# Optimization experiments

Measured on AMD Instinct MI355X. Metric: run time of the kernel, lower is better.

The kernel has to match this reference:

```python
import jax, jax.numpy as jnp
import numpy as np

C = 256
LN_EPS = 1e-5
LEAKY_SLOPE = 0.01

def _layernorm(t, g, b):
    mu = jnp.mean(t, axis=-1, keepdims=True)
    var = jnp.mean((t - mu) ** 2, axis=-1, keepdims=True)
    return (t - mu) * jax.lax.rsqrt(var + LN_EPS) * g + b

def setup_inputs() -> dict:
    key = jax.random.key(0)
    ks = jax.random.split(key, 16)
    b, d, h, w = 4, 4096, 64, 64
    s = lambda n: 1.0 / np.sqrt(n)
    return {
        "x": jax.random.normal(ks[0], (b, 1, d), jnp.float32),
        "y": jax.random.normal(ks[1], (b, C, h, w), jnp.float32),
        "q_w": jax.random.normal(ks[2], (C, C), jnp.float32) * s(C),
        "q_b": jnp.zeros((C,), jnp.float32),
        "dw_w": jax.random.normal(ks[3], (C,), jnp.float32),
        "dw_b": jnp.zeros((C,), jnp.float32),
        "kv_w1": jax.random.normal(ks[4], (1, C // 2), jnp.float32),
        "kv_b1": jnp.zeros((C // 2,), jnp.float32),
        "ln1_g": jnp.ones((C // 2,), jnp.float32),
        "ln1_b": jnp.zeros((C // 2,), jnp.float32),
        "kv_w2": jax.random.normal(ks[5], (C // 2, C), jnp.float32) * s(C // 2),
        "kv_b2": jnp.zeros((C,), jnp.float32),
        "ln2_g": jnp.ones((C,), jnp.float32),
        "ln2_b": jnp.zeros((C,), jnp.float32),
        "kv_w3": jax.random.normal(ks[6], (C, C), jnp.float32) * s(C),
        "kv_b3": jnp.zeros((C,), jnp.float32),
        "ln3_g": jnp.ones((C,), jnp.float32),
        "ln3_b": jnp.zeros((C,), jnp.float32),
        "kv_w4": jax.random.normal(ks[7], (C, 2 * C), jnp.float32) * s(C),
        "kv_b4": jnp.zeros((2 * C,), jnp.float32),
        "proj_w": jax.random.normal(ks[8], (C, C), jnp.float32) * s(C),
        "proj_b": jnp.zeros((C,), jnp.float32),
    }

def reference(x, y, q_w, q_b, dw_w, dw_b, kv_w1, kv_b1, ln1_g, ln1_b,
              kv_w2, kv_b2, ln2_g, ln2_b, kv_w3, kv_b3, ln3_g, ln3_b,
              kv_w4, kv_b4, proj_w, proj_b):
    b, c, h, w = y.shape
    # x: [b, 1, d] -> [b, d, 1]; MLP kv-generator lifts each scalar to 2c channels
    t = jnp.swapaxes(x, 1, 2)  # [b, d, 1]
    t = jax.nn.leaky_relu(_layernorm(t @ kv_w1 + kv_b1, ln1_g, ln1_b), LEAKY_SLOPE)
    t = jax.nn.leaky_relu(_layernorm(t @ kv_w2 + kv_b2, ln2_g, ln2_b), LEAKY_SLOPE)
    t = jax.nn.leaky_relu(_layernorm(t @ kv_w3 + kv_b3, ln3_g, ln3_b), LEAKY_SLOPE)
    t = jax.nn.silu(t @ kv_w4 + kv_b4)  # [b, d, 2c]
    k, v = jnp.split(t, 2, axis=-1)  # each [b, d, c]
    k = jnp.swapaxes(k, 1, 2)  # [b, c, d]
    # q = dwconv1x1(conv1x1(y)): 1x1 conv is a channel matmul; depthwise 1x1 is per-channel affine
    q = jnp.einsum('bchw,oc->bohw', y, q_w) + q_b[None, :, None, None]
    q = q * dw_w[None, :, None, None] + dw_b[None, :, None, None]
    q = q.reshape(b, c, h * w).transpose(0, 2, 1)  # [b, hw, c]
    scores = jnp.einsum('bic,bcd->bid', q, k) * (float(c) ** -0.5)  # [b, hw, d]
    attn = jax.nn.softmax(scores, axis=2)
    h_ = jnp.einsum('bid,bdc->bic', attn, v)  # [b, hw, c]
    h_ = h_.transpose(0, 2, 1).reshape(b, c, h, w)
    h_ = jnp.einsum('bchw,oc->bohw', h_, proj_w) + proj_b[None, :, None, None]
    return y + h_
```

## Files before the change

kernel.cpp:

```cpp
#include <hip/hip_runtime.h>
#include <cstdint>
#include <cstddef>

using bf16   = __bf16;
using bf16x8 = __bf16 __attribute__((ext_vector_type(8)));
using f32x4  = float  __attribute__((ext_vector_type(4)));
using u16    = unsigned short;
using ushort8 = __attribute__((ext_vector_type(8))) unsigned short;

#define MFMA16(a, b, c) __builtin_amdgcn_mfma_f32_16x16x32_bf16(a, b, c, 0, 0, 0)

__device__ __forceinline__ u16 f2bf(float f) {
  union { float f; unsigned u; } v; v.f = f;
  unsigned r = v.u + 0x7fffu + ((v.u >> 16) & 1u);
  return (u16)(r >> 16);
}
__device__ __forceinline__ u16 bfc(float f) {
  union { float f; unsigned u; } v; v.f = f;
  return (u16)((v.u + 0x8000u) >> 16);
}
__device__ __forceinline__ float b2f(u16 h) {
  union { unsigned u; float f; } v; v.u = ((unsigned)h) << 16; return v.f;
}
__device__ __forceinline__ bf16x8 ldb8(const u16* p) { return *(const bf16x8*)p; }
__device__ __forceinline__ float red_sum16(float v) {
  v += __shfl_xor(v, 1, 64); v += __shfl_xor(v, 2, 64);
  v += __shfl_xor(v, 4, 64); v += __shfl_xor(v, 8, 64);
  return v;
}
__device__ __forceinline__ void gll16(const u16* g, u16* l) {
  __builtin_amdgcn_global_load_lds(
      (const __attribute__((address_space(1))) void*)g,
      (__attribute__((address_space(3))) void*)l, 16, 0, 0);
}

#define QSCALE 0.09016844005556021f

__global__ void k_prep(const float* __restrict__ kv_w2, const float* __restrict__ kv_w3,
                       const float* __restrict__ kv_w4, const float* __restrict__ q_w,
                       const float* __restrict__ proj_w,
                       u16* __restrict__ Wt2, u16* __restrict__ Wt3, u16* __restrict__ Wt4,
                       u16* __restrict__ Qw, u16* __restrict__ Pww) {
  int idx = blockIdx.x * 256 + threadIdx.x;
  if (idx < 32768) {
    int n = idx >> 7, k = idx & 127;
    Wt2[idx] = f2bf(kv_w2[k * 256 + n]);
  } else if (idx < 98304) {
    int j = idx - 32768, n = j >> 8, k = j & 255;
    Wt3[j] = f2bf(kv_w3[k * 256 + n]);
  } else if (idx < 229376) {
    int j = idx - 98304, n = j >> 8, k = j & 255;
    Wt4[j] = f2bf(kv_w4[k * 512 + n]);
  } else if (idx < 294912) {
    int j = idx - 229376;
    Qw[j] = f2bf(q_w[j]);
  } else if (idx < 360448) {
    int j = idx - 294912;
    Pww[j] = f2bf(proj_w[j]);
  }
}

__device__ __forceinline__ void ln_store(f32x4* acc, const float* __restrict__ bias,
    const float* __restrict__ g, const float* __restrict__ bb, u16* act,
    int w, int quad, int l16) {
  #pragma unroll
  for (int f = 0; f < 16; ++f) {
    float bv = bias[f * 16 + l16];
    acc[f][0] += bv; acc[f][1] += bv; acc[f][2] += bv; acc[f][3] += bv;
  }
  #pragma unroll
  for (int r = 0; r < 4; ++r) {
    float s = 0;
    #pragma unroll
    for (int f = 0; f < 16; ++f) s += acc[f][r];
    s = red_sum16(s);
    float mu = s * (1.f / 256.f);
    float vv = 0;
    #pragma unroll
    for (int f = 0; f < 16; ++f) { float d = acc[f][r] - mu; vv += d * d; }
    vv = red_sum16(vv);
    float inv = rsqrtf(vv * (1.f / 256.f) + 1e-5f);
    int rl = w * 16 + quad * 4 + r;
    #pragma unroll
    for (int f = 0; f < 16; ++f) {
      int col = f * 16 + l16;
      float o = (acc[f][r] - mu) * inv * g[col] + bb[col];
      o = o > 0.f ? o : 0.01f * o;
      act[rl * 264 + col] = f2bf(o);
    }
  }
}

template<int K>
__device__ __forceinline__ void mlp_layer(u16* act, u16* sW, const u16* __restrict__ Wt,
    const float* __restrict__ bias, const float* __restrict__ g, const float* __restrict__ bb,
    int tid, int w, int quad, int l16) {
  bf16x8 af[K / 32];
  #pragma unroll
  for (int kk = 0; kk < K / 32; ++kk) af[kk] = ldb8(act + (w * 16 + l16) * 264 + kk * 32 + quad * 8);
  f32x4 z = {0.f, 0.f, 0.f, 0.f};
  f32x4 acc[16];
  #pragma unroll
  for (int f = 0; f < 16; ++f) acc[f] = z;
  for (int nc = 0; nc < 8; ++nc) {
    __syncthreads();
    #pragma unroll
    for (int p = 0; p < K / 64; ++p) {
      int q = p * 256 + tid; int row = q / (K / 8), c8 = q % (K / 8);
      *(uint4*)(sW + row * 264 + c8 * 8) = *(const uint4*)(Wt + (size_t)(nc * 32 + row) * K + c8 * 8);
    }
    __syncthreads();
    #pragma unroll
    for (int nb = 0; nb < 2; ++nb) {
      int f = nc * 2 + nb;
      #pragma unroll
      for (int kk = 0; kk < K / 32; ++kk)
        acc[f] = MFMA16(af[kk], ldb8(sW + (nb * 16 + l16) * 264 + kk * 32 + quad * 8), acc[f]);
    }
  }
  ln_store(acc, bias, g, bb, act, w, quad, l16);
  __syncthreads();
}

__device__ __forceinline__ void mlp_layer4(u16* act, u16* sW, const u16* __restrict__ Wt4,
    const float* __restrict__ bias4, u16* __restrict__ Kt, u16* __restrict__ Vt,
    int i0, int tid, int w, int quad, int l16) {
  bf16x8 af[8];
  #pragma unroll
  for (int kk = 0; kk < 8; ++kk) af[kk] = ldb8(act + (w * 16 + l16) * 264 + kk * 32 + quad * 8);
  f32x4 z = {0.f, 0.f, 0.f, 0.f};
  for (int h = 0; h < 2; ++h) {
    f32x4 acc[16];
    #pragma unroll
    for (int f = 0; f < 16; ++f) acc[f] = z;
    for (int nc = 0; nc < 8; ++nc) {
      __syncthreads();
      #pragma unroll
      for (int p = 0; p < 4; ++p) {
        int q = p * 256 + tid; int row = q >> 5, c8 = q & 31;
        *(uint4*)(sW + row * 264 + c8 * 8) =
            *(const uint4*)(Wt4 + (size_t)(h * 256 + nc * 32 + row) * 256 + c8 * 8);
      }
      __syncthreads();
      #pragma unroll
      for (int nb = 0; nb < 2; ++nb) {
        int f = nc * 2 + nb;
        #pragma unroll
        for (int kk = 0; kk < 8; ++kk)
          acc[f] = MFMA16(af[kk], ldb8(sW + (nb * 16 + l16) * 264 + kk * 32 + quad * 8), acc[f]);
      }
    }
    #pragma unroll
    for (int f = 0; f < 16; ++f) {
      int col = f * 16 + l16;
      float bv = bias4[h * 256 + col];
      if (h == 0) {
        int chunk = f * 2 + (l16 >> 3), co = col & 7;
        #pragma unroll
        for (int r = 0; r < 4; ++r) {
          int rowg = i0 + w * 16 + quad * 4 + r;
          float v = acc[f][r] + bv;
          v = v / (1.f + __expf(-v));
          int chs = (chunk + (rowg & 31)) & 31;
          Kt[(size_t)rowg * 256 + chs * 8 + co] = f2bf(v);
        }
      } else {
        int rowg0 = i0 + w * 16 + quad * 4;
        int bb2 = rowg0 >> 12, d0 = rowg0 & 4095;
        int dd = d0 & 31, qd = dd >> 3;
        int chs = (qd + (col & 3) + ((col >> 2) & 3)) & 3;
        ushort4 u;
        #pragma unroll
        for (int r = 0; r < 4; ++r) {
          float v = acc[f][r] + bv;
          v = v / (1.f + __expf(-v));
          ((u16*)&u)[r] = f2bf(v);
        }
        size_t off = ((size_t)(bb2 * 128 + (d0 >> 5)) * 8192) + col * 32 + chs * 8 + (dd & 7);
        *(ushort4*)(Vt + off) = u;
      }
    }
  }
}

__global__ __launch_bounds__(256, 2) void k_fused(
    const float* __restrict__ x, const float* __restrict__ w1, const float* __restrict__ bias1,
    const float* __restrict__ g1, const float* __restrict__ bb1,
    const u16* __restrict__ Wt2, const float* __restrict__ bias2,
    const float* __restrict__ g2, const float* __restrict__ bb2,
    const u16* __restrict__ Wt3, const float* __restrict__ bias3,
    const float* __restrict__ g3, const float* __restrict__ bb3,
    const u16* __restrict__ Wt4, const float* __restrict__ bias4,
    const float* __restrict__ y, const u16* __restrict__ Qw,
    const float* __restrict__ qb, const float* __restrict__ dww, const float* __restrict__ dwb,
    u16* __restrict__ Kt, u16* __restrict__ Vt, u16* __restrict__ Qb) {
  __shared__ __align__(16) u16 smem[25344];
  int tid = threadIdx.x, w = tid >> 6, lane = tid & 63, quad = lane >> 4, l16 = lane & 15;

  if (blockIdx.x < 256) {
    u16* act = smem;
    u16* sW  = smem + 16896;
    int i0 = blockIdx.x * 64;
    {
      int rloc = w * 16 + (lane >> 2);
      int c0 = (lane & 3) * 32;
      float xv = x[i0 + rloc];
      float t[32];
      float s = 0.f;
      #pragma unroll
      for (int j = 0; j < 32; ++j) { t[j] = xv * w1[c0 + j] + bias1[c0 + j]; s += t[j]; }
      s += __shfl_xor(s, 1, 64); s += __shfl_xor(s, 2, 64);
      float mu = s * (1.f / 128.f);
      float vv = 0.f;
      #pragma unroll
      for (int j = 0; j < 32; ++j) { float d = t[j] - mu; vv += d * d; }
      vv += __shfl_xor(vv, 1, 64); vv += __shfl_xor(vv, 2, 64);
      float inv = rsqrtf(vv * (1.f / 128.f) + 1e-5f);
      #pragma unroll
      for (int jo = 0; jo < 4; ++jo) {
        ushort8 pk;
        #pragma unroll
        for (int e = 0; e < 8; ++e) {
          int j = jo * 8 + e;
          float o = (t[j] - mu) * inv * g1[c0 + j] + bb1[c0 + j];
          o = o > 0.f ? o : 0.01f * o;
          pk[e] = f2bf(o);
        }
        *(ushort8*)(act + rloc * 264 + c0 + jo * 8) = pk;
      }
    }
    __syncthreads();
    mlp_layer<128>(act, sW, Wt2, bias2, g2, bb2, tid, w, quad, l16);
    mlp_layer<256>(act, sW, Wt3, bias3, g3, bb3, tid, w, quad, l16);
    mlp_layer4(act, sW, Wt4, bias4, Kt, Vt, i0, tid, w, quad, l16);
    return;
  }

  u16* sY = smem;
  u16* sB = smem + 4608;
  int t = blockIdx.x - 256;
  int b = t >> 6, i0 = (t & 63) * 64;
  f32x4 z = {0.f, 0.f, 0.f, 0.f};
  f32x4 acc[16];
  #pragma unroll
  for (int f = 0; f < 16; ++f) acc[f] = z;
  for (int kc = 0; kc < 4; ++kc) {
    if (kc) __syncthreads();
    {
      int cl = tid >> 4;
      int il = (tid & 15) * 4;
      #pragma unroll
      for (int p = 0; p < 4; ++p) {
        int c = kc * 64 + p * 16 + cl;
        float4 v = *(const float4*)(y + ((size_t)(b * 256 + c)) * 4096 + i0 + il);
        sY[(il + 0) * 72 + p * 16 + cl] = f2bf(v.x);
        sY[(il + 1) * 72 + p * 16 + cl] = f2bf(v.y);
        sY[(il + 2) * 72 + p * 16 + cl] = f2bf(v.z);
        sY[(il + 3) * 72 + p * 16 + cl] = f2bf(v.w);
      }
    }
    #pragma unroll
    for (int p = 0; p < 8; ++p) {
      int q = p * 256 + tid; int row = q >> 3, k8 = q & 7;
      *(uint4*)(sB + row * 72 + k8 * 8) = *(const uint4*)(Qw + (size_t)row * 256 + kc * 64 + k8 * 8);
    }
    __syncthreads();
    #pragma unroll
    for (int kk = 0; kk < 2; ++kk) {
      bf16x8 af = ldb8(sY + (w * 16 + l16) * 72 + kk * 32 + quad * 8);
      #pragma unroll
      for (int f = 0; f < 16; ++f) {
        bf16x8 bfr = ldb8(sB + (f * 16 + l16) * 72 + kk * 32 + quad * 8);
        acc[f] = MFMA16(af, bfr, acc[f]);
      }
    }
  }
  #pragma unroll
  for (int f = 0; f < 16; ++f) {
    int col = f * 16 + l16;
    float q0 = qb[col], sc = dww[col], dB = dwb[col];
    #pragma unroll
    for (int r = 0; r < 4; ++r) {
      int rowg = i0 + w * 16 + quad * 4 + r;
      float v = ((acc[f][r] + q0) * sc + dB) * QSCALE;
      Qb[((size_t)(b * 4096 + rowg)) * 256 + col] = f2bf(v);
    }
  }
}

__global__ __launch_bounds__(256, 2) void k_attn(const u16* __restrict__ Qb, const u16* __restrict__ Kt,
    const u16* __restrict__ Vt, u16* __restrict__ Op, float* __restrict__ Ol) {
  __shared__ __align__(16) u16 smem[37888];
  int tid = threadIdx.x, w = tid >> 6, lane = tid & 63, quad = lane >> 4, l16 = lane & 15;
  int b = blockIdx.x & 3, kh = (blockIdx.x >> 2) & 3, qt = blockIdx.x >> 4;
  int i0 = qt * 128 + w * 32;

  bf16x8 qf[2][8];
  {
    const u16* qrow = Qb + ((size_t)(b * 4096 + i0 + l16)) * 256 + quad * 8;
    #pragma unroll
    for (int kk = 0; kk < 8; ++kk) {
      qf[0][kk] = ldb8(qrow + kk * 32);
      qf[1][kk] = ldb8(qrow + 16 * 256 + kk * 32);
    }
  }
  f32x4 z = {0.f, 0.f, 0.f, 0.f};
  f32x4 oacc[2][16];
  #pragma unroll
  for (int sub = 0; sub < 2; ++sub)
    #pragma unroll
    for (int f = 0; f < 16; ++f) oacc[sub][f] = z;
  float l4[2][4] = {{0.f, 0.f, 0.f, 0.f}, {0.f, 0.f, 0.f, 0.f}};

  u16* sPw = smem + 32768 + w * 1280;
  int wp = w & 1;
  const u16* gSrc = ((w < 2) ? Kt : Vt) + ((size_t)(b * 128 + kh * 32) * 8192) + wp * 4096 + lane * 8;
  u16* lBase = smem + ((w < 2) ? 0 : 8192) + wp * 4096 + lane * 8;

  #pragma unroll
  for (int i = 0; i < 8; ++i) gll16(gSrc + i * 512, lBase + i * 512);
  gSrc += 8192;

  #pragma unroll 1
  for (int kt = 0; kt < 32; ++kt) {
    int buf = kt & 1;
    const u16* sK = smem + buf * 16384;
    const u16* sV = sK + 8192;
    asm volatile("s_waitcnt vmcnt(0)" ::: "memory");
    __syncthreads();
    if (kt < 31) {
      u16* dst = lBase + (buf ^ 1) * 16384;
      #pragma unroll
      for (int i = 0; i < 8; ++i) gll16(gSrc + i * 512, dst + i * 512);
      gSrc += 8192;
    }
    f32x4 s00 = z, s01 = z, s10 = z, s11 = z;
    #pragma unroll
    for (int kk = 0; kk < 8; ++kk) {
      int ch0 = (kk * 4 + quad + l16) & 31;
      int ch1 = (ch0 + 16) & 31;
      bf16x8 k0 = ldb8(sK + l16 * 256 + ch0 * 8);
      bf16x8 k1 = ldb8(sK + (16 + l16) * 256 + ch1 * 8);
      s00 = MFMA16(qf[0][kk], k0, s00);
      s01 = MFMA16(qf[0][kk], k1, s01);
      s10 = MFMA16(qf[1][kk], k0, s10);
      s11 = MFMA16(qf[1][kk], k1, s11);
    }
    #pragma unroll
    for (int r = 0; r < 4; ++r) {
      float p0 = exp2f(s00[r]);
      float p1 = exp2f(s01[r]);
      float p2 = exp2f(s10[r]);
      float p3 = exp2f(s11[r]);
      l4[0][r] += p0 + p1;
      l4[1][r] += p2 + p3;
      int row0 = (quad * 4 + r) * 40;
      sPw[row0 + l16]            = bfc(p0);
      sPw[row0 + 16 + l16]       = bfc(p1);
      sPw[640 + row0 + l16]      = bfc(p2);
      sPw[640 + row0 + 16 + l16] = bfc(p3);
    }
    asm volatile("s_waitcnt lgkmcnt(0)" ::: "memory");
    bf16x8 pf0 = ldb8(sPw + l16 * 40 + quad * 8);
    bf16x8 pf1 = ldb8(sPw + 640 + l16 * 40 + quad * 8);
    #pragma unroll
    for (int f = 0; f < 16; ++f) {
      int c = f * 16 + l16;
      int chs = (quad + (c & 3) + ((c >> 2) & 3)) & 3;
      bf16x8 vf = ldb8(sV + c * 32 + chs * 8);
      oacc[0][f] = MFMA16(pf0, vf, oacc[0][f]);
      oacc[1][f] = MFMA16(pf1, vf, oacc[1][f]);
    }
  }
  #pragma unroll
  for (int sub = 0; sub < 2; ++sub)
    #pragma unroll
    for (int r = 0; r < 4; ++r) l4[sub][r] = red_sum16(l4[sub][r]);
  #pragma unroll
  for (int sub = 0; sub < 2; ++sub)
    #pragma unroll
    for (int r = 0; r < 4; ++r) {
      size_t gr = (size_t)kh * 16384 + b * 4096 + i0 + sub * 16 + quad * 4 + r;
      u16* orow = Op + gr * 256;
      #pragma unroll
      for (int f = 0; f < 16; ++f) orow[f * 16 + l16] = f2bf(oacc[sub][f][r]);
      if (l16 == 0) Ol[gr] = l4[sub][r];
    }
}

__global__ __launch_bounds__(256) void k_proj(const u16* __restrict__ Op, const float* __restrict__ Ol,
    const u16* __restrict__ Pw, const float* __restrict__ pb, const float* __restrict__ y,
    float* __restrict__ out) {
  __shared__ u16 sA[64 * 136];
  __shared__ u16 sB[64 * 136];
  __shared__ float sW[64];
  int tid = threadIdx.x, w = tid >> 6, lane = tid & 63, quad = lane >> 4, l16 = lane & 15;
  int i0 = blockIdx.x * 64, o0 = blockIdx.y * 64, b = blockIdx.z;
  if (tid < 64) {
    size_t gr = (size_t)b * 4096 + i0 + tid;
    float L = Ol[gr] + Ol[gr + 16384] + Ol[gr + 32768] + Ol[gr + 49152];
    sW[tid] = 1.f / L;
  }
  __syncthreads();
  f32x4 z = {0.f, 0.f, 0.f, 0.f};
  f32x4 acc[4] = {z, z, z, z};
  for (int kc = 0; kc < 2; ++kc) {
    if (kc) __syncthreads();
    #pragma unroll
    for (int p = 0; p < 4; ++p) {
      int q = p * 256 + tid; int row = q >> 4, c8 = q & 15;
      *(uint4*)(sA + row * 136 + c8 * 8) = *(const uint4*)(Pw + ((size_t)(o0 + row)) * 256 + kc * 128 + c8 * 8);
      size_t gr = (size_t)b * 4096 + i0 + row;
      const u16* hp = Op + gr * 256 + kc * 128 + c8 * 8;
      uint4 u0 = *(const uint4*)(hp);
      uint4 u1 = *(const uint4*)(hp + 4194304);
      uint4 u2 = *(const uint4*)(hp + 8388608);
      uint4 u3 = *(const uint4*)(hp + 12582912);
      float wr = sW[row];
      const u16* p0 = (const u16*)&u0; const u16* p1 = (const u16*)&u1;
      const u16* p2 = (const u16*)&u2; const u16* p3 = (const u16*)&u3;
      ushort8 ov;
      #pragma unroll
      for (int e = 0; e < 8; ++e) {
        float v = (b2f(p0[e]) + b2f(p1[e]) + b2f(p2[e]) + b2f(p3[e])) * wr;
        ov[e] = f2bf(v);
      }
      *(ushort8*)(sB + row * 136 + c8 * 8) = ov;
    }
    __syncthreads();
    #pragma unroll
    for (int kk = 0; kk < 4; ++kk) {
      bf16x8 af = ldb8(sA + (w * 16 + l16) * 136 + kk * 32 + quad * 8);
      #pragma unroll
      for (int nb = 0; nb < 4; ++nb) {
        bf16x8 bfr = ldb8(sB + (nb * 16 + l16) * 136 + kk * 32 + quad * 8);
        acc[nb] = MFMA16(af, bfr, acc[nb]);
      }
    }
  }
  #pragma unroll
  for (int nb = 0; nb < 4; ++nb) {
    #pragma unroll
    for (int r = 0; r < 4; ++r) {
      int og = o0 + w * 16 + quad * 4 + r;
      size_t idx = ((size_t)(b * 256 + og)) * 4096 + i0 + nb * 16 + l16;
      out[idx] = y[idx] + acc[nb][r] + pb[og];
    }
  }
}

extern "C" void kernel_launch(void* const* d_in, const int* in_sizes, int n_in,
                              void* d_out, int out_size, void* d_ws, size_t ws_size,
                              hipStream_t stream) {
  (void)in_sizes; (void)n_in; (void)out_size; (void)ws_size;
  const float* x     = (const float*)d_in[0];
  const float* y     = (const float*)d_in[1];
  const float* q_w   = (const float*)d_in[2];
  const float* q_b   = (const float*)d_in[3];
  const float* dw_w  = (const float*)d_in[4];
  const float* dw_b  = (const float*)d_in[5];
  const float* kv_w1 = (const float*)d_in[6];
  const float* kv_b1 = (const float*)d_in[7];
  const float* ln1_g = (const float*)d_in[8];
  const float* ln1_b = (const float*)d_in[9];
  const float* kv_w2 = (const float*)d_in[10];
  const float* kv_b2 = (const float*)d_in[11];
  const float* ln2_g = (const float*)d_in[12];
  const float* ln2_b = (const float*)d_in[13];
  const float* kv_w3 = (const float*)d_in[14];
  const float* kv_b3 = (const float*)d_in[15];
  const float* ln3_g = (const float*)d_in[16];
  const float* ln3_b = (const float*)d_in[17];
  const float* kv_w4 = (const float*)d_in[18];
  const float* kv_b4 = (const float*)d_in[19];
  const float* proj_w = (const float*)d_in[20];
  const float* proj_b = (const float*)d_in[21];
  float* out = (float*)d_out;
  unsigned char* ws = (unsigned char*)d_ws;

  u16* Wt2 = (u16*)(ws + 0);
  u16* Wt3 = (u16*)(ws + 65536);
  u16* Wt4 = (u16*)(ws + 196608);
  u16* Qw  = (u16*)(ws + 458752);
  u16* Pww = (u16*)(ws + 589824);
  u16* Qb  = (u16*)(ws + 9437184);
  u16* Kt  = (u16*)(ws + 17825792);
  u16* Vt  = (u16*)(ws + 26214400);
  u16* Op  = (u16*)(ws + 34603008);
  float* Ol = (float*)(ws + 68157440);

  k_prep<<<1408, 256, 0, stream>>>(kv_w2, kv_w3, kv_w4, q_w, proj_w, Wt2, Wt3, Wt4, Qw, Pww);
  k_fused<<<512, 256, 0, stream>>>(x, kv_w1, kv_b1, ln1_g, ln1_b,
                                   Wt2, kv_b2, ln2_g, ln2_b,
                                   Wt3, kv_b3, ln3_g, ln3_b,
                                   Wt4, kv_b4,
                                   y, Qw, q_b, dw_w, dw_b,
                                   Kt, Vt, Qb);
  k_attn<<<512, 256, 0, stream>>>(Qb, Kt, Vt, Op, Ol);
  k_proj<<<dim3(64, 4, 4), 256, 0, stream>>>(Op, Ol, Pww, proj_b, y, out);
}
```

Baseline: 266.8 us.

## Simplify V tile layout, add MFMA priority hints, widen proj output tile

```diff
diff --git a/kernel.cpp b/kernel.cpp
--- a/kernel.cpp
+++ b/kernel.cpp
@@ -166,9 +166,10 @@
         }
       } else {
         int rowg0 = i0 + w * 16 + quad * 4;
-        int bb2 = rowg0 >> 12, d0 = rowg0 & 4095;
-        int dd = d0 & 31, qd = dd >> 3;
-        int chs = (qd + (col & 3) + ((col >> 2) & 3)) & 3;
+        int bb2 = rowg0 >> 12;
+        int tt = (rowg0 >> 5) & 127;
+        int qv = (rowg0 >> 3) & 3;
+        int e0 = rowg0 & 7;
         ushort4 u;
         #pragma unroll
         for (int r = 0; r < 4; ++r) {
@@ -176,7 +177,7 @@
           v = v / (1.f + __expf(-v));
           ((u16*)&u)[r] = f2bf(v);
         }
-        size_t off = ((size_t)(bb2 * 128 + (d0 >> 5)) * 8192) + col * 32 + chs * 8 + (dd & 7);
+        size_t off = ((size_t)(bb2 * 128 + tt)) * 8192 + f * 512 + qv * 128 + l16 * 8 + e0;
         *(ushort4*)(Vt + off) = u;
       }
     }
@@ -335,6 +336,7 @@
       gSrc += 8192;
     }
     f32x4 s00 = z, s01 = z, s10 = z, s11 = z;
+    __builtin_amdgcn_s_setprio(1);
     #pragma unroll
     for (int kk = 0; kk < 8; ++kk) {
       int ch0 = (kk * 4 + quad + l16) & 31;
@@ -346,6 +348,7 @@
       s10 = MFMA16(qf[1][kk], k0, s10);
       s11 = MFMA16(qf[1][kk], k1, s11);
     }
+    __builtin_amdgcn_s_setprio(0);
     #pragma unroll
     for (int r = 0; r < 4; ++r) {
       float p0 = exp2f(s00[r]);
@@ -363,14 +366,15 @@
     asm volatile("s_waitcnt lgkmcnt(0)" ::: "memory");
     bf16x8 pf0 = ldb8(sPw + l16 * 40 + quad * 8);
     bf16x8 pf1 = ldb8(sPw + 640 + l16 * 40 + quad * 8);
+    const u16* vbase = sV + lane * 8;
+    __builtin_amdgcn_s_setprio(1);
     #pragma unroll
     for (int f = 0; f < 16; ++f) {
-      int c = f * 16 + l16;
-      int chs = (quad + (c & 3) + ((c >> 2) & 3)) & 3;
-      bf16x8 vf = ldb8(sV + c * 32 + chs * 8);
+      bf16x8 vf = ldb8(vbase + f * 512);
       oacc[0][f] = MFMA16(pf0, vf, oacc[0][f]);
       oacc[1][f] = MFMA16(pf1, vf, oacc[1][f]);
     }
+    __builtin_amdgcn_s_setprio(0);
   }
   #pragma unroll
   for (int sub = 0; sub < 2; ++sub)
@@ -391,11 +395,11 @@
 __global__ __launch_bounds__(256) void k_proj(const u16* __restrict__ Op, const float* __restrict__ Ol,
     const u16* __restrict__ Pw, const float* __restrict__ pb, const float* __restrict__ y,
     float* __restrict__ out) {
-  __shared__ u16 sA[64 * 136];
-  __shared__ u16 sB[64 * 136];
+  __shared__ __align__(16) u16 sA[128 * 136];
+  __shared__ __align__(16) u16 sB[64 * 136];
   __shared__ float sW[64];
   int tid = threadIdx.x, w = tid >> 6, lane = tid & 63, quad = lane >> 4, l16 = lane & 15;
-  int i0 = blockIdx.x * 64, o0 = blockIdx.y * 64, b = blockIdx.z;
+  int i0 = blockIdx.x * 64, o0 = blockIdx.y * 128, b = blockIdx.z;
   if (tid < 64) {
     size_t gr = (size_t)b * 4096 + i0 + tid;
     float L = Ol[gr] + Ol[gr + 16384] + Ol[gr + 32768] + Ol[gr + 49152];
@@ -403,13 +407,17 @@
   }
   __syncthreads();
   f32x4 z = {0.f, 0.f, 0.f, 0.f};
-  f32x4 acc[4] = {z, z, z, z};
+  f32x4 acc[2][4] = {{z, z, z, z}, {z, z, z, z}};
   for (int kc = 0; kc < 2; ++kc) {
     if (kc) __syncthreads();
     #pragma unroll
+    for (int p = 0; p < 8; ++p) {
+      int q = p * 256 + tid; int row = q >> 4, c8 = q & 15;
+      *(uint4*)(sA + row * 136 + c8 * 8) = *(const uint4*)(Pw + ((size_t)(o0 + row)) * 256 + kc * 128 + c8 * 8);
+    }
+    #pragma unroll
     for (int p = 0; p < 4; ++p) {
       int q = p * 256 + tid; int row = q >> 4, c8 = q & 15;
-      *(uint4*)(sA + row * 136 + c8 * 8) = *(const uint4*)(Pw + ((size_t)(o0 + row)) * 256 + kc * 128 + c8 * 8);
       size_t gr = (size_t)b * 4096 + i0 + row;
       const u16* hp = Op + gr * 256 + kc * 128 + c8 * 8;
       uint4 u0 = *(const uint4*)(hp);
@@ -430,23 +438,26 @@
     __syncthreads();
     #pragma unroll
     for (int kk = 0; kk < 4; ++kk) {
-      bf16x8 af = ldb8(sA + (w * 16 + l16) * 136 + kk * 32 + quad * 8);
+      bf16x8 af0 = ldb8(sA + (w * 16 + l16) * 136 + kk * 32 + quad * 8);
+      bf16x8 af1 = ldb8(sA + (64 + w * 16 + l16) * 136 + kk * 32 + quad * 8);
       #pragma unroll
       for (int nb = 0; nb < 4; ++nb) {
         bf16x8 bfr = ldb8(sB + (nb * 16 + l16) * 136 + kk * 32 + quad * 8);
-        acc[nb] = MFMA16(af, bfr, acc[nb]);
-      }
-    }
-  }
-  #pragma unroll
-  for (int nb = 0; nb < 4; ++nb) {
-    #pragma unroll
-    for (int r = 0; r < 4; ++r) {
-      int og = o0 + w * 16 + quad * 4 + r;
-      size_t idx = ((size_t)(b * 256 + og)) * 4096 + i0 + nb * 16 + l16;
-      out[idx] = y[idx] + acc[nb][r] + pb[og];
-    }
-  }
+        acc[0][nb] = MFMA16(af0, bfr, acc[0][nb]);
+        acc[1][nb] = MFMA16(af1, bfr, acc[1][nb]);
+      }
+    }
+  }
+  #pragma unroll
+  for (int oc = 0; oc < 2; ++oc)
+    #pragma unroll
+    for (int nb = 0; nb < 4; ++nb)
+      #pragma unroll
+      for (int r = 0; r < 4; ++r) {
+        int og = o0 + oc * 64 + w * 16 + quad * 4 + r;
+        size_t idx = ((size_t)(b * 256 + og)) * 4096 + i0 + nb * 16 + l16;
+        out[idx] = y[idx] + acc[oc][nb][r] + pb[og];
+      }
 }
 
 extern "C" void kernel_launch(void* const* d_in, const int* in_sizes, int n_in,
@@ -497,5 +508,5 @@
                                    y, Qw, q_b, dw_w, dw_b,
                                    Kt, Vt, Qb);
   k_attn<<<512, 256, 0, stream>>>(Qb, Kt, Vt, Op, Ol);
-  k_proj<<<dim3(64, 4, 4), 256, 0, stream>>>(Op, Ol, Pww, proj_b, y, out);
-}
+  k_proj<<<dim3(64, 2, 4), 256, 0, stream>>>(Op, Ol, Pww, proj_b, y, out);
+}
```

After: 262.6 us. About the same (-1.6%).
